# Kernel optimization log

Hardware: AMD Instinct MI355X
Metric: run time of the kernel (lower is better)

## Reference

```python
import jax, jax.numpy as jnp
import numpy as np

DEPTH = 4
HEADS = 4
DH = 32          # dim_head
DIM = 256
INNER = HEADS * DH
B, N, E = 1, 20000, 320000
LN_EPS = 1e-5


def _layernorm(x, g, b):
    mu = jnp.mean(x, axis=-1, keepdims=True)
    var = jnp.var(x, axis=-1, keepdims=True)  # biased, matches torch LayerNorm
    return (x - mu) * jax.lax.rsqrt(var + LN_EPS) * g + b


def setup_inputs() -> dict:
    key = jax.random.key(0)
    ks = jax.random.split(key, 20)
    x = jax.random.normal(ks[0], (B, N, DIM), jnp.float32)
    edge_index = jax.random.randint(ks[1], (2, E), 0, N)

    s = 0.02
    inp = {
        "x": x,
        "edge_index": edge_index,
        "ln1_g": jnp.ones((DEPTH, DIM), jnp.float32),
        "ln1_b": jnp.zeros((DEPTH, DIM), jnp.float32),
        "wq": jax.random.normal(ks[2], (DEPTH, INNER, DIM), jnp.float32) * s,
        "bq": jnp.zeros((DEPTH, INNER), jnp.float32),
        "wk": jax.random.normal(ks[3], (DEPTH, INNER, DIM), jnp.float32) * s,
        "bk": jnp.zeros((DEPTH, INNER), jnp.float32),
        "wv": jax.random.normal(ks[4], (DEPTH, INNER, DIM), jnp.float32) * s,
        "bv": jnp.zeros((DEPTH, INNER), jnp.float32),
        "wo": jax.random.normal(ks[5], (DEPTH, DIM, INNER), jnp.float32) * s,
        "bo": jnp.zeros((DEPTH, DIM), jnp.float32),
        "ln2_g": jnp.ones((DEPTH, DIM), jnp.float32),
        "ln2_b": jnp.zeros((DEPTH, DIM), jnp.float32),
        "w1": jax.random.normal(ks[6], (DEPTH, 4 * DIM, DIM), jnp.float32) * s,
        "b1": jnp.zeros((DEPTH, 4 * DIM), jnp.float32),
        "w2": jax.random.normal(ks[7], (DEPTH, DIM, 4 * DIM), jnp.float32) * s,
        "b2": jnp.zeros((DEPTH, DIM), jnp.float32),
    }
    return inp


def _graph_transformer(x, edge_index, ln1_g, ln1_b, wq, bq, wk, bk, wv, bv,
                       wo, bo, ln2_g, ln2_b, w1, b1, w2, b2):
    src = edge_index[0]  # j (messages flow j -> i)
    dst = edge_index[1]  # i
    scale = 1.0 / np.sqrt(DH).astype(np.float32)
    for l in range(DEPTH):
        # --- GraphAttention ---
        h = _layernorm(x, ln1_g[l], ln1_b[l])                     # (B,N,D)
        def proj(w, b):
            p = h @ w.T + b                                        # (B,N,INNER)
            return jnp.moveaxis(p, 0, 1).reshape(N, B, HEADS, DH)  # (N,B,H,Dh)
        q = proj(wq[l], bq[l])
        k = proj(wk[l], bk[l])
        v = proj(wv[l], bv[l])
        q_i = q[dst]                                               # (E,B,H,Dh)
        k_j = k[src]
        v_j = v[src]
        alpha = jnp.sum(q_i * k_j, axis=-1) * scale                # (E,B,H)
        # segment softmax over destination node per (B, head)
        amax = jax.ops.segment_max(alpha, dst, num_segments=N)     # (N,B,H)
        ex = jnp.exp(alpha - amax[dst])
        denom = jax.ops.segment_sum(ex, dst, num_segments=N)       # (N,B,H)
        w_attn = ex / (denom[dst] + 1e-16)                         # (E,B,H)
        agg = jax.ops.segment_sum(v_j * w_attn[..., None], dst,
                                  num_segments=N)                  # (N,B,H,Dh)
        out = jnp.moveaxis(agg.reshape(N, B, INNER), 0, 1)         # (B,N,INNER)
        out = out @ wo[l].T + bo[l]                                # (B,N,D)
        x = out + x
        # --- FeedForward ---
        h2 = _layernorm(x, ln2_g[l], ln2_b[l])
        ff = jax.nn.gelu(h2 @ w1[l].T + b1[l], approximate=False) @ w2[l].T + b2[l]
        x = ff + x
    return x


def reference(x, edge_index, ln1_g, ln1_b, wq, bq, wk, bk, wv, bv,
              wo, bo, ln2_g, ln2_b, w1, b1, w2, b2):
    return _graph_transformer(x, edge_index, ln1_g, ln1_b, wq, bq, wk, bk,
                              wv, bv, wo, bo, ln2_g, ln2_b, w1, b1, w2, b2)
```

## Files before the change

kernel.cpp:

```cpp
#include <hip/hip_runtime.h>
#include <hip/hip_bf16.h>
#include <math.h>

#define DIMC 256
#define INNERC 128
#define HEADSC 4
#define DHC 32
#define QKVC 384

typedef __attribute__((ext_vector_type(8))) short bf16frag;
typedef __attribute__((ext_vector_type(4))) float f32x4;

__device__ __forceinline__ float gelu_exact(float x) {
    return 0.5f * x * (1.0f + erff(x * 0.70710678118654752f));
}

__device__ __forceinline__ float b2f(short s) {
    return __uint_as_float(((unsigned)(unsigned short)s) << 16);
}

__device__ __forceinline__ void gload_lds16(const void* g, void* l) {
    __builtin_amdgcn_global_load_lds(
        (const __attribute__((address_space(1))) void*)g,
        (__attribute__((address_space(3))) void*)l, 16, 0, 0);
}

__global__ __launch_bounds__(256)
void ln_kernel(const float* __restrict__ x, const float* __restrict__ g,
               const float* __restrict__ b, __hip_bfloat16* __restrict__ out,
               int N)
{
    int row = blockIdx.x * 4 + (threadIdx.x >> 6);
    if (row >= N) return;
    int lane = threadIdx.x & 63;
    float4 v = *(const float4*)(x + (size_t)row * DIMC + lane * 4);
    float s = v.x + v.y + v.z + v.w;
    float s2 = v.x * v.x + v.y * v.y + v.z * v.z + v.w * v.w;
#pragma unroll
    for (int off = 32; off; off >>= 1) {
        s += __shfl_xor(s, off);
        s2 += __shfl_xor(s2, off);
    }
    float mean = s * (1.f / DIMC);
    float var = s2 * (1.f / DIMC) - mean * mean;
    float rs = rsqrtf(var + 1e-5f);
    float4 gv = *(const float4*)(g + lane * 4);
    float4 bv = *(const float4*)(b + lane * 4);
    __hip_bfloat16 o[4];
    o[0] = __float2bfloat16((v.x - mean) * rs * gv.x + bv.x);
    o[1] = __float2bfloat16((v.y - mean) * rs * gv.y + bv.y);
    o[2] = __float2bfloat16((v.z - mean) * rs * gv.z + bv.z);
    o[3] = __float2bfloat16((v.w - mean) * rs * gv.w + bv.w);
    *(short4*)(out + (size_t)row * DIMC + lane * 4) = *(short4*)o;
}

__global__ void f2b_kernel(const float* __restrict__ src,
                           __hip_bfloat16* __restrict__ dst, int n)
{
    int i = (blockIdx.x * blockDim.x + threadIdx.x) * 4;
    if (i < n) {
        float4 v = *(const float4*)(src + i);
        dst[i + 0] = __float2bfloat16(v.x);
        dst[i + 1] = __float2bfloat16(v.y);
        dst[i + 2] = __float2bfloat16(v.z);
        dst[i + 3] = __float2bfloat16(v.w);
    }
}

__global__ __launch_bounds__(256)
void packqkv_kernel(const float* __restrict__ wq, const float* __restrict__ wk,
                    const float* __restrict__ wv, const float* __restrict__ bq,
                    const float* __restrict__ bk, const float* __restrict__ bv,
                    __hip_bfloat16* __restrict__ wqkv, float* __restrict__ bqkv)
{
    int row = blockIdx.x;
    int l = row / QKVC, c = row % QKVC;
    int which = c >> 7, cc = c & 127;
    const float* srcw = which == 0 ? wq : which == 1 ? wk : wv;
    const float* srcb = which == 0 ? bq : which == 1 ? bk : bv;
    srcw += ((size_t)l * INNERC + cc) * DIMC;
    wqkv[(size_t)row * DIMC + threadIdx.x] = __float2bfloat16(srcw[threadIdx.x]);
    if (threadIdx.x == 0) bqkv[row] = srcb[l * INNERC + cc];
}

template<int EPI>
__global__ __launch_bounds__(512)
void mfma_gemm(const __hip_bfloat16* __restrict__ A,
               const __hip_bfloat16* __restrict__ W,
               const float* __restrict__ bias, const float* __restrict__ res,
               void* __restrict__ Cout, int M, int K, int OUT,
               int mtiles, int ntiles)
{
    constexpr int ASZ = 128 * 128;
    constexpr int WSZ = 128 * 128;
    __shared__ char lds[2 * ASZ + 2 * WSZ];

    int nwg = mtiles * ntiles;
    int orig = blockIdx.x;
    int q = nwg >> 3, r = nwg & 7;
    int xcd = orig & 7, loc = orig >> 3;
    int wgid = (xcd < r ? xcd * (q + 1) : r * (q + 1) + (xcd - r) * q) + loc;
    int bm = (wgid / ntiles) * 128;
    int bn = (wgid % ntiles) * 128;

    int tid = threadIdx.x;
    int lane = tid & 63;
    int w = tid >> 6;
    int wr = w >> 2, wc = w & 3;
    int l15 = lane & 15, l4 = lane >> 4;

    f32x4 acc[4][2] = {};

    auto stage = [&](int t, int b) {
        int k0 = t * 64;
        char* Asb = lds + b * ASZ;
        char* Wsb = lds + 2 * ASZ + b * WSZ;
#pragma unroll
        for (int it = 0; it < 2; ++it) {
            int chunk = it * 512 + tid;
            int rr = chunk >> 3;
            int sc = (chunk & 7) ^ (rr & 7);
            int grow = min(bm + rr, M - 1);
            gload_lds16((const char*)A + ((size_t)grow * K + k0) * 2 + sc * 16,
                        Asb + chunk * 16);
        }
#pragma unroll
        for (int it = 0; it < 2; ++it) {
            int chunk = it * 512 + tid;
            int rr = chunk >> 3;
            int sc = (chunk & 7) ^ (rr & 7);
            gload_lds16((const char*)W + ((size_t)(bn + rr) * K + k0) * 2 + sc * 16,
                        Wsb + chunk * 16);
        }
    };

    int nk = K >> 6;
    stage(0, 0);
    for (int t = 0; t < nk; ++t) {
        int cur = t & 1;
        if (t + 1 < nk) {
            stage(t + 1, cur ^ 1);
            asm volatile("s_waitcnt vmcnt(4)" ::: "memory");
        } else {
            asm volatile("s_waitcnt vmcnt(0)" ::: "memory");
        }
        __builtin_amdgcn_s_barrier();
        char* As = lds + cur * ASZ;
        char* Ws = lds + 2 * ASZ + cur * WSZ;
#pragma unroll
        for (int s = 0; s < 2; ++s) {
            bf16frag af[4], bfr[2];
            int kb = s * 64 + (l4 << 4);
#pragma unroll
            for (int m = 0; m < 4; ++m) {
                int ar = wr * 64 + m * 16 + l15;
                af[m] = *(const bf16frag*)(As + ar * 128 + (kb ^ ((ar & 7) << 4)));
            }
#pragma unroll
            for (int n = 0; n < 2; ++n) {
                int br = wc * 32 + n * 16 + l15;
                bfr[n] = *(const bf16frag*)(Ws + br * 128 + (kb ^ ((br & 7) << 4)));
            }
#pragma unroll
            for (int m = 0; m < 4; ++m)
#pragma unroll
                for (int n = 0; n < 2; ++n)
                    acc[m][n] = __builtin_amdgcn_mfma_f32_16x16x32_bf16(
                        af[m], bfr[n], acc[m][n], 0, 0, 0);
        }
        __builtin_amdgcn_s_barrier();
    }

#pragma unroll
    for (int m = 0; m < 4; ++m)
#pragma unroll
        for (int rr = 0; rr < 4; ++rr) {
            int grow = bm + wr * 64 + m * 16 + (l4 << 2) + rr;
            if (grow < M) {
#pragma unroll
                for (int n = 0; n < 2; ++n) {
                    int gcol = bn + wc * 32 + n * 16 + l15;
                    float val = acc[m][n][rr] + bias[gcol];
                    if (EPI == 1) val = gelu_exact(val);
                    if (EPI == 2) {
                        val += res[(size_t)grow * OUT + gcol];
                        ((float*)Cout)[(size_t)grow * OUT + gcol] = val;
                    } else {
                        ((__hip_bfloat16*)Cout)[(size_t)grow * OUT + gcol] =
                            __float2bfloat16(val);
                    }
                }
            }
        }
}

__global__ void count_kernel(const int* __restrict__ dst, int* __restrict__ count, int E)
{
    int e = blockIdx.x * blockDim.x + threadIdx.x;
    if (e < E) atomicAdd(&count[dst[e]], 1);
}

__global__ __launch_bounds__(1024)
void scanA_kernel(const int* __restrict__ count, int* __restrict__ rowptr,
                  int* __restrict__ bsum, int N)
{
    __shared__ int sdata[1024];
    int b = blockIdx.x, t = threadIdx.x;
    int idx = b * 1024 + t;
    int v = (idx < N) ? count[idx] : 0;
    sdata[t] = v;
    __syncthreads();
    for (int off = 1; off < 1024; off <<= 1) {
        int add = (t >= off) ? sdata[t - off] : 0;
        __syncthreads();
        sdata[t] += add;
        __syncthreads();
    }
    if (idx < N) rowptr[idx + 1] = sdata[t];
    if (t == 1023) bsum[b] = sdata[1023];
}

__global__ void scanB_kernel(int* __restrict__ bsum, int nb)
{
    int t = threadIdx.x;
    int v = (t < nb) ? bsum[t] : 0;
#pragma unroll
    for (int off = 1; off < 64; off <<= 1) {
        int u = __shfl_up(v, off);
        if (t >= off) v += u;
    }
    if (t < nb) bsum[t] = v;
}

__global__ __launch_bounds__(1024)
void scanC_kernel(int* __restrict__ rowptr, const int* __restrict__ bsum, int N)
{
    int b = blockIdx.x, t = threadIdx.x;
    int idx = b * 1024 + t;
    if (idx == 0) rowptr[0] = 0;
    if (idx < N && b > 0) rowptr[idx + 1] += bsum[b - 1];
}

__global__ void scatter_kernel(const int* __restrict__ src, const int* __restrict__ dst,
                               const int* __restrict__ rowptr, int* __restrict__ cursor,
                               int* __restrict__ srcperm, int E)
{
    int e = blockIdx.x * blockDim.x + threadIdx.x;
    if (e < E) {
        int d = dst[e];
        int pos = rowptr[d] + atomicAdd(&cursor[d], 1);
        srcperm[pos] = src[e];
    }
}

__global__ __launch_bounds__(256)
void attn_kernel(const __hip_bfloat16* __restrict__ qkv, const int* __restrict__ rowptr,
                 const int* __restrict__ srcperm, __hip_bfloat16* __restrict__ agg,
                 int N)
{
    int wid = (blockIdx.x * 256 + threadIdx.x) >> 6;
    if (wid >= N) return;
    int lane = threadIdx.x & 63;
    int h = lane >> 4, u = lane & 15;
    int i = wid;
    int beg = rowptr[i], deg = rowptr[i + 1] - beg;
    const short* base = (const short*)qkv;
    const float scale = 0.17677669529663687f;

    bf16frag qf[4];
    const short* qr = base + (size_t)i * QKVC + h * 32;
#pragma unroll
    for (int c = 0; c < 4; ++c) qf[c] = *(const bf16frag*)(qr + c * 8);

    float m_run = -3.4e38f, d_run = 0.f;
    float accx = 0.f, accy = 0.f;

    int j = (u < deg) ? srcperm[beg + u] : i;
    bf16frag kf[4];
    {
        const short* kr = base + (size_t)j * QKVC + 128 + h * 32;
#pragma unroll
        for (int c = 0; c < 4; ++c) kf[c] = *(const bf16frag*)(kr + c * 8);
    }

    for (int c0 = 0; c0 < deg; c0 += 16) {
        int cn = min(16, deg - c0);
        bool valid = (u < cn);

        int nxt = c0 + 16 + u;
        int jn = (nxt < deg) ? srcperm[beg + nxt] : i;

        float dot = 0.f;
#pragma unroll
        for (int c = 0; c < 4; ++c)
#pragma unroll
            for (int e = 0; e < 8; ++e)
                dot += b2f(qf[c][e]) * b2f(kf[c][e]);
        float alpha = valid ? dot * scale : -3.4e38f;

        float cm = alpha;
#pragma unroll
        for (int off = 8; off; off >>= 1) cm = fmaxf(cm, __shfl_xor(cm, off));
        float m_new = fmaxf(m_run, cm);
        float rescale = __expf(m_run - m_new);
        float w = valid ? __expf(alpha - m_new) : 0.f;
        float dsum = w;
#pragma unroll
        for (int off = 8; off; off >>= 1) dsum += __shfl_xor(dsum, off);
        d_run = d_run * rescale + dsum;
        m_run = m_new;
        accx *= rescale;
        accy *= rescale;

        bf16frag kfn[4];
        {
            const short* krn = base + (size_t)jn * QKVC + 128 + h * 32;
#pragma unroll
            for (int c = 0; c < 4; ++c) kfn[c] = *(const bf16frag*)(krn + c * 8);
        }

        float wes[16];
        unsigned vws[16];
#pragma unroll
        for (int e = 0; e < 16; ++e) {
            wes[e] = __shfl(w, h * 16 + e);
            int je = __shfl(j, h * 16 + e);
            vws[e] = *(const unsigned*)(base + (size_t)je * QKVC + 256 + h * 32 + u * 2);
        }
#pragma unroll
        for (int e = 0; e < 16; ++e) {
            accx += wes[e] * b2f((short)(vws[e] & 0xffff));
            accy += wes[e] * b2f((short)(vws[e] >> 16));
        }
        j = jn;
#pragma unroll
        for (int c = 0; c < 4; ++c) kf[c] = kfn[c];
    }

    float inv = 1.f / (d_run + 1e-16f);
    __hip_bfloat16* outp = agg + (size_t)i * INNERC + h * 32 + u * 2;
    outp[0] = __float2bfloat16(accx * inv);
    outp[1] = __float2bfloat16(accy * inv);
}

extern "C" void kernel_launch(void* const* d_in, const int* in_sizes, int n_in,
                              void* d_out, int out_size, void* d_ws, size_t ws_size,
                              hipStream_t stream)
{
    const float* x    = (const float*)d_in[0];
    const int*   ei   = (const int*)  d_in[1];
    const float* ln1g = (const float*)d_in[2];
    const float* ln1b = (const float*)d_in[3];
    const float* wq   = (const float*)d_in[4];
    const float* bq   = (const float*)d_in[5];
    const float* wk   = (const float*)d_in[6];
    const float* bk   = (const float*)d_in[7];
    const float* wv   = (const float*)d_in[8];
    const float* bv   = (const float*)d_in[9];
    const float* wo   = (const float*)d_in[10];
    const float* bo   = (const float*)d_in[11];
    const float* ln2g = (const float*)d_in[12];
    const float* ln2b = (const float*)d_in[13];
    const float* w1   = (const float*)d_in[14];
    const float* b1   = (const float*)d_in[15];
    const float* w2   = (const float*)d_in[16];
    const float* b2   = (const float*)d_in[17];

    const int N = in_sizes[0] / DIMC;
    const int E = in_sizes[1] / 2;
    const int* srcIdx = ei;
    const int* dstIdx = ei + E;

    char* p = (char*)d_ws;
    auto alloc = [&](size_t bytes) {
        char* r = p;
        p += (bytes + 255) & ~(size_t)255;
        return r;
    };
    float*          xbuf   = (float*)alloc((size_t)N * DIMC * 4);
    __hip_bfloat16* h      = (__hip_bfloat16*)alloc((size_t)N * DIMC * 2);
    __hip_bfloat16* qkv    = (__hip_bfloat16*)alloc((size_t)N * QKVC * 2);
    __hip_bfloat16* agg    = (__hip_bfloat16*)alloc((size_t)N * INNERC * 2);
    __hip_bfloat16* u      = (__hip_bfloat16*)alloc((size_t)N * 1024 * 2);
    int*            rowptr = (int*)alloc((size_t)(N + 1) * 4);
    int*            cnt    = (int*)alloc((size_t)N * 4);
    int*            bsum   = (int*)alloc((size_t)64 * 4);
    int*            srcperm= (int*)alloc((size_t)E * 4);
    __hip_bfloat16* wqkvB  = (__hip_bfloat16*)alloc((size_t)4 * QKVC * DIMC * 2);
    float*          bqkvF  = (float*)alloc((size_t)4 * QKVC * 4);
    __hip_bfloat16* woB    = (__hip_bfloat16*)alloc((size_t)4 * DIMC * INNERC * 2);
    __hip_bfloat16* w1B    = (__hip_bfloat16*)alloc((size_t)4 * 1024 * DIMC * 2);
    __hip_bfloat16* w2B    = (__hip_bfloat16*)alloc((size_t)4 * DIMC * 1024 * 2);

    packqkv_kernel<<<4 * QKVC, 256, 0, stream>>>(wq, wk, wv, bq, bk, bv, wqkvB, bqkvF);
    {
        int n = 4 * DIMC * INNERC;
        f2b_kernel<<<(n / 4 + 255) / 256, 256, 0, stream>>>(wo, woB, n);
        n = 4 * 1024 * DIMC;
        f2b_kernel<<<(n / 4 + 255) / 256, 256, 0, stream>>>(w1, w1B, n);
        f2b_kernel<<<(n / 4 + 255) / 256, 256, 0, stream>>>(w2, w2B, n);
    }

    int nb = (N + 1023) / 1024;
    hipMemsetAsync(cnt, 0, (size_t)N * 4, stream);
    count_kernel<<<(E + 255) / 256, 256, 0, stream>>>(dstIdx, cnt, E);
    scanA_kernel<<<nb, 1024, 0, stream>>>(cnt, rowptr, bsum, N);
    scanB_kernel<<<1, 64, 0, stream>>>(bsum, nb);
    scanC_kernel<<<nb, 1024, 0, stream>>>(rowptr, bsum, N);
    hipMemsetAsync(cnt, 0, (size_t)N * 4, stream);
    scatter_kernel<<<(E + 255) / 256, 256, 0, stream>>>(srcIdx, dstIdx, rowptr, cnt, srcperm, E);

    int mt = (N + 127) / 128;
    int lnBlocks = (N + 3) / 4;
    int attnBlocks = (N * 64 + 255) / 256;
    for (int l = 0; l < 4; ++l) {
        const float* xin = (l == 0) ? x : xbuf;
        ln_kernel<<<lnBlocks, 256, 0, stream>>>(xin, ln1g + l * DIMC, ln1b + l * DIMC, h, N);
        mfma_gemm<0><<<mt * 3, 512, 0, stream>>>(
            h, wqkvB + (size_t)l * QKVC * DIMC, bqkvF + l * QKVC, nullptr,
            qkv, N, DIMC, QKVC, mt, 3);
        attn_kernel<<<attnBlocks, 256, 0, stream>>>(qkv, rowptr, srcperm, agg, N);
        mfma_gemm<2><<<mt * 2, 512, 0, stream>>>(
            agg, woB + (size_t)l * DIMC * INNERC, bo + l * DIMC, xin,
            xbuf, N, INNERC, DIMC, mt, 2);
        ln_kernel<<<lnBlocks, 256, 0, stream>>>(xbuf, ln2g + l * DIMC, ln2b + l * DIMC, h, N);
        mfma_gemm<1><<<mt * 8, 512, 0, stream>>>(
            h, w1B + (size_t)l * 1024 * DIMC, b1 + l * 1024, nullptr,
            u, N, DIMC, 1024, mt, 8);
        float* xout = (l == 3) ? (float*)d_out : xbuf;
        mfma_gemm<2><<<mt * 2, 512, 0, stream>>>(
            u, w2B + (size_t)l * DIMC * 1024, b2 + l * DIMC, xbuf,
            xout, N, 1024, DIMC, mt, 2);
    }
}
```

Before: 545.7 us.

## Fuse LayerNorm into residual output GEMMs with full-row 64x256 tiles

```diff
diff --git a/kernel.cpp b/kernel.cpp
--- a/kernel.cpp
+++ b/kernel.cpp
@@ -190,6 +190,163 @@
                             __float2bfloat16(val);
                     }
                 }
+            }
+        }
+}
+
+template<int K>
+__global__ __launch_bounds__(512)
+void gemm_ln(const __hip_bfloat16* __restrict__ A,
+             const __hip_bfloat16* __restrict__ W,
+             const float* __restrict__ bias, const float* __restrict__ res,
+             float* __restrict__ outF,
+             const float* __restrict__ lnG, const float* __restrict__ lnB,
+             __hip_bfloat16* __restrict__ hOut,
+             int M, int mtiles, int doLN)
+{
+    constexpr int ASZ = 64 * 128;
+    constexpr int WSZ = 256 * 128;
+    __shared__ char lds[2 * ASZ + 2 * WSZ];
+
+    int orig = blockIdx.x;
+    int q = mtiles >> 3, r = mtiles & 7;
+    int xcd = orig & 7, loc = orig >> 3;
+    int wgid = (xcd < r ? xcd * (q + 1) : r * (q + 1) + (xcd - r) * q) + loc;
+    int bm = wgid * 64;
+
+    int tid = threadIdx.x;
+    int lane = tid & 63;
+    int wc = tid >> 6;
+    int l15 = lane & 15, l4 = lane >> 4;
+
+    f32x4 acc[4][2] = {};
+
+    auto stage = [&](int t, int b) {
+        int k0 = t * 64;
+        char* Asb = lds + b * ASZ;
+        char* Wsb = lds + 2 * ASZ + b * WSZ;
+        {
+            int chunk = tid;
+            int rr = chunk >> 3;
+            int sc = (chunk & 7) ^ (rr & 7);
+            int grow = min(bm + rr, M - 1);
+            gload_lds16((const char*)A + ((size_t)grow * K + k0) * 2 + sc * 16,
+                        Asb + chunk * 16);
+        }
+#pragma unroll
+        for (int it = 0; it < 4; ++it) {
+            int chunk = it * 512 + tid;
+            int rr = chunk >> 3;
+            int sc = (chunk & 7) ^ (rr & 7);
+            gload_lds16((const char*)W + ((size_t)rr * K + k0) * 2 + sc * 16,
+                        Wsb + chunk * 16);
+        }
+    };
+
+    int nk = K >> 6;
+    stage(0, 0);
+    for (int t = 0; t < nk; ++t) {
+        int cur = t & 1;
+        if (t + 1 < nk) {
+            stage(t + 1, cur ^ 1);
+            asm volatile("s_waitcnt vmcnt(5)" ::: "memory");
+        } else {
+            asm volatile("s_waitcnt vmcnt(0)" ::: "memory");
+        }
+        __builtin_amdgcn_s_barrier();
+        char* As = lds + cur * ASZ;
+        char* Ws = lds + 2 * ASZ + cur * WSZ;
+#pragma unroll
+        for (int s = 0; s < 2; ++s) {
+            bf16frag af[4], bfr[2];
+            int kb = s * 64 + (l4 << 4);
+#pragma unroll
+            for (int m = 0; m < 4; ++m) {
+                int ar = m * 16 + l15;
+                af[m] = *(const bf16frag*)(As + ar * 128 + (kb ^ ((ar & 7) << 4)));
+            }
+#pragma unroll
+            for (int n = 0; n < 2; ++n) {
+                int br = wc * 32 + n * 16 + l15;
+                bfr[n] = *(const bf16frag*)(Ws + br * 128 + (kb ^ ((br & 7) << 4)));
+            }
+#pragma unroll
+            for (int m = 0; m < 4; ++m)
+#pragma unroll
+                for (int n = 0; n < 2; ++n)
+                    acc[m][n] = __builtin_amdgcn_mfma_f32_16x16x32_bf16(
+                        af[m], bfr[n], acc[m][n], 0, 0, 0);
+        }
+        __builtin_amdgcn_s_barrier();
+    }
+
+    float* wsum = (float*)lds;
+    float* wsq  = wsum + 512;
+    float* muA  = wsq + 512;
+    float* rsA  = muA + 64;
+
+#pragma unroll
+    for (int m = 0; m < 4; ++m)
+#pragma unroll
+        for (int rr = 0; rr < 4; ++rr) {
+            int lrow = m * 16 + (l4 << 2) + rr;
+            int grow = bm + lrow;
+            float v0 = 0.f, v1 = 0.f;
+            if (grow < M) {
+                int c0 = wc * 32 + l15;
+                int c1 = c0 + 16;
+                v0 = acc[m][0][rr] + bias[c0] + res[(size_t)grow * 256 + c0];
+                v1 = acc[m][1][rr] + bias[c1] + res[(size_t)grow * 256 + c1];
+                outF[(size_t)grow * 256 + c0] = v0;
+                outF[(size_t)grow * 256 + c1] = v1;
+                acc[m][0][rr] = v0;
+                acc[m][1][rr] = v1;
+            }
+            if (doLN) {
+                float ps = v0 + v1;
+                float pq = v0 * v0 + v1 * v1;
+#pragma unroll
+                for (int off = 8; off; off >>= 1) {
+                    ps += __shfl_xor(ps, off);
+                    pq += __shfl_xor(pq, off);
+                }
+                if (l15 == 0) {
+                    wsum[wc * 64 + lrow] = ps;
+                    wsq[wc * 64 + lrow] = pq;
+                }
+            }
+        }
+
+    if (!doLN) return;
+    __syncthreads();
+    if (tid < 64) {
+        float s = 0.f, q2 = 0.f;
+#pragma unroll
+        for (int w8 = 0; w8 < 8; ++w8) {
+            s += wsum[w8 * 64 + tid];
+            q2 += wsq[w8 * 64 + tid];
+        }
+        float m_ = s * (1.f / 256.f);
+        float va = q2 * (1.f / 256.f) - m_ * m_;
+        muA[tid] = m_;
+        rsA[tid] = rsqrtf(va + 1e-5f);
+    }
+    __syncthreads();
+
+#pragma unroll
+    for (int m = 0; m < 4; ++m)
+#pragma unroll
+        for (int rr = 0; rr < 4; ++rr) {
+            int lrow = m * 16 + (l4 << 2) + rr;
+            int grow = bm + lrow;
+            if (grow < M) {
+                float mu = muA[lrow], rs = rsA[lrow];
+                int c0 = wc * 32 + l15;
+                int c1 = c0 + 16;
+                hOut[(size_t)grow * 256 + c0] =
+                    __float2bfloat16((acc[m][0][rr] - mu) * rs * lnG[c0] + lnB[c0]);
+                hOut[(size_t)grow * 256 + c1] =
+                    __float2bfloat16((acc[m][1][rr] - mu) * rs * lnG[c1] + lnB[c1]);
             }
         }
 }
@@ -411,25 +568,27 @@
     scatter_kernel<<<(E + 255) / 256, 256, 0, stream>>>(srcIdx, dstIdx, rowptr, cnt, srcperm, E);
 
     int mt = (N + 127) / 128;
-    int lnBlocks = (N + 3) / 4;
+    int mt64 = (N + 63) / 64;
     int attnBlocks = (N * 64 + 255) / 256;
     for (int l = 0; l < 4; ++l) {
         const float* xin = (l == 0) ? x : xbuf;
-        ln_kernel<<<lnBlocks, 256, 0, stream>>>(xin, ln1g + l * DIMC, ln1b + l * DIMC, h, N);
+        if (l == 0)
+            ln_kernel<<<(N + 3) / 4, 256, 0, stream>>>(x, ln1g, ln1b, h, N);
         mfma_gemm<0><<<mt * 3, 512, 0, stream>>>(
             h, wqkvB + (size_t)l * QKVC * DIMC, bqkvF + l * QKVC, nullptr,
             qkv, N, DIMC, QKVC, mt, 3);
         attn_kernel<<<attnBlocks, 256, 0, stream>>>(qkv, rowptr, srcperm, agg, N);
-        mfma_gemm<2><<<mt * 2, 512, 0, stream>>>(
+        gemm_ln<128><<<mt64, 512, 0, stream>>>(
             agg, woB + (size_t)l * DIMC * INNERC, bo + l * DIMC, xin,
-            xbuf, N, INNERC, DIMC, mt, 2);
-        ln_kernel<<<lnBlocks, 256, 0, stream>>>(xbuf, ln2g + l * DIMC, ln2b + l * DIMC, h, N);
+            xbuf, ln2g + l * DIMC, ln2b + l * DIMC, h, N, mt64, 1);
         mfma_gemm<1><<<mt * 8, 512, 0, stream>>>(
             h, w1B + (size_t)l * 1024 * DIMC, b1 + l * 1024, nullptr,
             u, N, DIMC, 1024, mt, 8);
         float* xout = (l == 3) ? (float*)d_out : xbuf;
-        mfma_gemm<2><<<mt * 2, 512, 0, stream>>>(
+        gemm_ln<1024><<<mt64, 512, 0, stream>>>(
             u, w2B + (size_t)l * DIMC * 1024, b2 + l * DIMC, xbuf,
-            xout, N, 1024, DIMC, mt, 2);
-    }
-}
+            xout, ln1g + (size_t)(l + 1 < 4 ? l + 1 : 0) * DIMC,
+            ln1b + (size_t)(l + 1 < 4 ? l + 1 : 0) * DIMC, h, N, mt64,
+            (l < 3) ? 1 : 0);
+    }
+}
```

Result: slower. 569.7 us (+4.4%).
